# Optimization experiments

Measured on AMD Instinct MI355X. Metric: run time of the kernel, lower is better.

Reference implementation:

```python
import jax, jax.numpy as jnp
import numpy as np

B, S, HID = 8, 1024, 1024
NH, HD = 16, 64  # num heads, head dim
EPS = 1e-12


def setup_inputs() -> dict:
    key = jax.random.key(0)
    ks = jax.random.split(key, 8)
    sc = 0.02
    return {
        "hidden_states": jax.random.normal(ks[0], (B, S, HID), jnp.float32),
        "attention_mask": jnp.zeros((B, 1, 1, S), jnp.bool_),
        "rel_pos": jax.random.normal(ks[1], (1, NH, S, S), jnp.float32),
        "rel_2d_pos": jax.random.normal(ks[2], (1, NH, S, S), jnp.float32),
        "w_qkv": jax.random.normal(ks[3], (3 * HID, HID), jnp.float32) * sc,
        "q_bias": jnp.zeros((1, 1, HID), jnp.float32),
        "v_bias": jnp.zeros((1, 1, HID), jnp.float32),
        "w_out": jax.random.normal(ks[4], (HID, HID), jnp.float32) * sc,
        "b_out": jnp.zeros((HID,), jnp.float32),
        "ln_gamma": jnp.ones((HID,), jnp.float32),
        "ln_beta": jnp.zeros((HID,), jnp.float32),
    }


def reference(hidden_states, attention_mask, rel_pos, rel_2d_pos,
              w_qkv, q_bias, v_bias, w_out, b_out, ln_gamma, ln_beta):
    x = hidden_states
    # fast_qkv: single projection, no bias; then add q_bias/v_bias
    qkv = jnp.einsum('bsh,oh->bso', x, w_qkv)  # [B,S,3*HID]
    q, k, v = jnp.split(qkv, 3, axis=-1)
    q = q + q_bias
    v = v + v_bias
    # [B,S,HID] -> [B,NH,S,HD]
    to_heads = lambda t: t.reshape(B, S, NH, HD).transpose(0, 2, 1, 3)
    qh, kh, vh = to_heads(q), to_heads(k), to_heads(v)
    qh = qh / jnp.sqrt(jnp.float32(HD))
    scores = jnp.einsum('bhqd,bhkd->bhqk', qh, kh)
    scores = scores + rel_pos + rel_2d_pos
    scores = jnp.where(attention_mask, -jnp.inf, scores.astype(jnp.float32))
    probs = jax.nn.softmax(scores, axis=-1).astype(vh.dtype)
    ctx = jnp.einsum('bhqk,bhkd->bhqd', probs, vh)
    ctx = ctx.transpose(0, 2, 1, 3).reshape(B, S, HID)
    # self-output: dense + residual + LayerNorm
    h = jnp.einsum('bsh,oh->bso', ctx, w_out) + b_out + x
    mu = jnp.mean(h, axis=-1, keepdims=True)
    var = jnp.var(h, axis=-1, keepdims=True)
    out = (h - mu) / jnp.sqrt(var + EPS) * ln_gamma + ln_beta
    return out
```

## Files before the change

### kernel.cpp

```cpp
#include <hip/hip_runtime.h>
#include <stdint.h>
#include <stddef.h>

typedef unsigned short u16;
typedef __attribute__((ext_vector_type(8))) short short8;
typedef __attribute__((ext_vector_type(4))) float f32x4;
typedef __attribute__((ext_vector_type(4))) unsigned short ushort4v;
typedef __attribute__((ext_vector_type(4))) unsigned char uchar4v;
typedef __attribute__((ext_vector_type(2))) unsigned int uint2v;

constexpr int B_ = 8, S_ = 1024, HID_ = 1024, NH_ = 16, HD_ = 64;
#define LOG2E_F 1.4426950408889634f
#define QSCALE_F 0.18033688011112043f
#define SHIFT2_F 11.541560327111707f

__device__ __forceinline__ u16 f2b(float f) {
  unsigned int u = __builtin_bit_cast(unsigned int, f);
  u += 0x7fff + ((u >> 16) & 1);
  return (u16)(u >> 16);
}
__device__ __forceinline__ float b2f(u16 s) {
  unsigned int u = ((unsigned int)s) << 16;
  return __builtin_bit_cast(float, u);
}
__device__ __forceinline__ float fexp2(float x) {
#if __has_builtin(__builtin_amdgcn_exp2f)
  return __builtin_amdgcn_exp2f(x);
#else
  return exp2f(x);
#endif
}
__device__ __forceinline__ void llds16(const void* g, void* l) {
  __builtin_amdgcn_global_load_lds((__attribute__((address_space(1))) void*)g,
                                   (__attribute__((address_space(3))) void*)l, 16, 0, 0);
}

__global__ __launch_bounds__(256) void prep_cvt(
    const float* __restrict__ x, const float* __restrict__ wqkv,
    const float* __restrict__ wout, u16* __restrict__ xb,
    u16* __restrict__ wqkvb, u16* __restrict__ woutb) {
  const int NX8 = B_ * S_ * HID_ / 8, NW18 = 3 * HID_ * HID_ / 8, NW28 = HID_ * HID_ / 8;
  const int tot = NX8 + NW18 + NW28;
  for (int i = blockIdx.x * blockDim.x + threadIdx.x; i < tot; i += gridDim.x * blockDim.x) {
    const float4* s; u16* d; int j;
    if (i < NX8)              { s = (const float4*)x;    d = xb;    j = i; }
    else if (i < NX8 + NW18)  { s = (const float4*)wqkv; d = wqkvb; j = i - NX8; }
    else                      { s = (const float4*)wout; d = woutb; j = i - NX8 - NW18; }
    float4 v0 = s[2 * (size_t)j], v1 = s[2 * (size_t)j + 1];
    short8 o;
    o[0] = (short)f2b(v0.x); o[1] = (short)f2b(v0.y);
    o[2] = (short)f2b(v0.z); o[3] = (short)f2b(v0.w);
    o[4] = (short)f2b(v1.x); o[5] = (short)f2b(v1.y);
    o[6] = (short)f2b(v1.z); o[7] = (short)f2b(v1.w);
    *(short8*)(d + 8 * (size_t)j) = o;
  }
}

__global__ __launch_bounds__(256) void gemm_qkv(
    const u16* __restrict__ W, const u16* __restrict__ X,
    const float* __restrict__ qbias, const float* __restrict__ vbias,
    u16* __restrict__ Qb, u16* __restrict__ Kb, u16* __restrict__ Vtb) {
  constexpr int K = HID_;
  __shared__ u16 smem[128 * 136];
  u16* Ws0 = smem;
  u16* Ws1 = smem + 4096;
  u16* Xs0 = smem + 8192;
  u16* Xs1 = smem + 12288;
  const int lin = blockIdx.x;
  const int virt = (lin & 7) * 192 + (lin >> 3);
  const int o0 = (virt % 24) * 128, s0 = (virt / 24) * 128;
  const int t = threadIdx.x, lane = t & 63, wv = t >> 6;
  const int wr = wv >> 1, wc = wv & 1, ln = lane & 15, q8 = lane >> 4;
  f32x4 acc[4][4] = {};

  for (int kt = 0; kt < K / 64; ++kt) {
    const int k0 = kt * 64;
#pragma unroll
    for (int c = 0; c < 2; ++c) {
      int idx = c * 256 + t, row = idx >> 2, cc = (idx & 3) * 8;
      const int db = (c * 256 + wv * 64) * 8;
      llds16(W + (size_t)(o0 + row) * K + k0 + cc,      Ws0 + db);
      llds16(W + (size_t)(o0 + row) * K + k0 + 32 + cc, Ws1 + db);
      llds16(X + (size_t)(s0 + row) * K + k0 + cc,      Xs0 + db);
      llds16(X + (size_t)(s0 + row) * K + k0 + 32 + cc, Xs1 + db);
    }
    __syncthreads();
#pragma unroll
    for (int hh = 0; hh < 2; ++hh) {
      const u16* Wh = hh ? Ws1 : Ws0;
      const u16* Xh = hh ? Xs1 : Xs0;
      short8 of[4], sf[4];
#pragma unroll
      for (int mi = 0; mi < 4; ++mi)
        of[mi] = *(const short8*)(Wh + (wr * 64 + mi * 16 + ln) * 32 + q8 * 8);
#pragma unroll
      for (int ni = 0; ni < 4; ++ni)
        sf[ni] = *(const short8*)(Xh + (wc * 64 + ni * 16 + ln) * 32 + q8 * 8);
#pragma unroll
      for (int mi = 0; mi < 4; ++mi)
#pragma unroll
        for (int ni = 0; ni < 4; ++ni)
          acc[mi][ni] = __builtin_amdgcn_mfma_f32_16x16x32_bf16(of[mi], sf[ni], acc[mi][ni], 0, 0, 0);
    }
    __syncthreads();
  }

  const int sec = o0 >> 10;

  if (sec == 2) {
#pragma unroll
    for (int mi = 0; mi < 4; ++mi) {
      const int ocol = wr * 64 + mi * 16 + q8 * 4;
      const int oo = (o0 + ocol) & 1023;
      float4 b4 = *(const float4*)(vbias + oo);
#pragma unroll
      for (int ni = 0; ni < 4; ++ni) {
        const int srow = wc * 64 + ni * 16 + ln;
#pragma unroll
        for (int r = 0; r < 4; ++r)
          smem[(ocol + r) * 136 + srow] = f2b(acc[mi][ni][r] + ((const float*)&b4)[r]);
      }
    }
    __syncthreads();
#pragma unroll
    for (int i = 0; i < 8; ++i) {
      int flat = i * 256 + t;
      int dl = flat >> 4, s8 = (flat & 15) * 8;
      short8 v = *(const short8*)(smem + dl * 136 + s8);
      int oo = (o0 + dl) & 1023, hh = oo >> 6, dd = oo & 63;
      int bb = s0 >> 10, ss = (s0 + s8) & 1023;
      *(short8*)(Vtb + ((size_t)(bb * NH_ + hh) * HD_ + dd) * S_ + ss) = v;
    }
    return;
  }

#pragma unroll
  for (int mi = 0; mi < 4; ++mi) {
    const int ocol = wr * 64 + mi * 16 + q8 * 4;
    const int oo = (o0 + ocol) & 1023;
    float4 b4;
    if (sec == 0) b4 = *(const float4*)(qbias + oo);
    else          b4 = float4{0.f, 0.f, 0.f, 0.f};
#pragma unroll
    for (int ni = 0; ni < 4; ++ni) {
      const int srow = wc * 64 + ni * 16 + ln;
      u16 e[4];
#pragma unroll
      for (int r = 0; r < 4; ++r) {
        float v = acc[mi][ni][r] + ((const float*)&b4)[r];
        if (sec == 0) v *= QSCALE_F;
        e[r] = f2b(v);
      }
      uint2v pw;
      pw[0] = (unsigned)e[0] | ((unsigned)e[1] << 16);
      pw[1] = (unsigned)e[2] | ((unsigned)e[3] << 16);
      *(uint2v*)(smem + srow * 136 + ocol) = pw;
    }
  }
  __syncthreads();
  u16* dst = (sec == 0) ? Qb : Kb;
#pragma unroll
  for (int i = 0; i < 8; ++i) {
    int flat = i * 256 + t;
    int srow = flat >> 4, c8 = (flat & 15) * 8;
    short8 v = *(const short8*)(smem + srow * 136 + c8);
    int oo = (o0 + c8) & 1023, hh = oo >> 6, dd = oo & 63;
    int s = s0 + srow, bb = s >> 10, ss = s & 1023;
    *(short8*)(dst + ((size_t)(bb * NH_ + hh) * S_ + ss) * HD_ + dd) = v;
  }
}

__global__ __launch_bounds__(512, 2) void flash_attn(
    const u16* __restrict__ Qb, const u16* __restrict__ Kb,
    const u16* __restrict__ Vtb, const float* __restrict__ relp,
    const float* __restrict__ rel2,
    const unsigned char* __restrict__ mask, u16* __restrict__ ctxb) {
  const int lin = blockIdx.x;
  const int virt = (lin & 7) * 64 + (lin >> 3);
  const int h = virt >> 5, qt_blk = (virt >> 3) & 3, b = virt & 7;
  const int bh = b * NH_ + h, q0 = qt_blk * 256;
  const int t = threadIdx.x, lane = t & 63, wv = t >> 6;
  const int ln = lane & 15, q8 = lane >> 4;

  __shared__ u16 smem[28160];
  u16* Ks  = smem;
  u16* Vts = smem + 9216;
  u16* Pw  = smem + 17920 + wv * 1280;

  const int krow = t >> 3, kcol = (t & 7) * 8;
  const int vrow = t >> 4, vcol = (t & 15) * 8;

  const float* relA = relp + ((size_t)h * S_ + q0 + wv * 32 + ln) * S_;
  const float* relB = rel2 + ((size_t)h * S_ + q0 + wv * 32 + ln) * S_;

  short8 kreg[2], vreg[2];
#pragma unroll
  for (int i = 0; i < 2; ++i)
    kreg[i] = *(const short8*)(Kb + ((size_t)bh * S_ + i * 64 + krow) * HD_ + kcol);
#pragma unroll
  for (int i = 0; i < 2; ++i)
    vreg[i] = *(const short8*)(Vtb + ((size_t)bh * HD_ + i * 32 + vrow) * S_ + vcol);

  short8 qf[2][2];
#pragma unroll
  for (int qt = 0; qt < 2; ++qt)
#pragma unroll
    for (int kc = 0; kc < 2; ++kc)
      qf[qt][kc] = *(const short8*)(Qb + ((size_t)bh * S_ + q0 + wv * 32 + qt * 16 + ln) * HD_ + kc * 32 + q8 * 8);

  f32x4 Oa[4][2] = {};
  float rs2[2] = {0.f, 0.f};

  for (int kt128 = 0; kt128 < 8; ++kt128) {
    const int k0 = kt128 * 128;

    uchar4v mg[4][2];
#pragma unroll
    for (int kvc = 0; kvc < 4; ++kvc)
#pragma unroll
      for (int sub = 0; sub < 2; ++sub)
        mg[kvc][sub] = *(const uchar4v*)(mask + b * S_ + k0 + (kvc * 2 + sub) * 16 + q8 * 4);

    __syncthreads();
#pragma unroll
    for (int i = 0; i < 2; ++i)
      *(short8*)(Ks + (i * 64 + krow) * 72 + kcol) = kreg[i];
#pragma unroll
    for (int i = 0; i < 2; ++i)
      *(short8*)(Vts + (i * 32 + vrow) * 136 + vcol) = vreg[i];
    if (kt128 < 7) {
      const int k0n = k0 + 128;
#pragma unroll
      for (int i = 0; i < 2; ++i)
        kreg[i] = *(const short8*)(Kb + ((size_t)bh * S_ + k0n + i * 64 + krow) * HD_ + kcol);
#pragma unroll
      for (int i = 0; i < 2; ++i)
        vreg[i] = *(const short8*)(Vtb + ((size_t)bh * HD_ + i * 32 + vrow) * S_ + k0n + vcol);
    }
    __syncthreads();

#pragma unroll
    for (int kvc = 0; kvc < 4; ++kvc) {
#pragma unroll
      for (int sub = 0; sub < 2; ++sub) {
        const int kt = kvc * 2 + sub;
        const int kg = k0 + kt * 16 + q8 * 4;
        short8 kf0 = *(const short8*)(Ks + (kt * 16 + ln) * 72 + q8 * 8);
        short8 kf1 = *(const short8*)(Ks + (kt * 16 + ln) * 72 + 32 + q8 * 8);
        uchar4v m4 = mg[kvc][sub];
        f32x4 mbase;
#pragma unroll
        for (int r = 0; r < 4; ++r) mbase[r] = (m4[r] ? -1e30f : 0.f) - SHIFT2_F;
#pragma unroll
        for (int qt = 0; qt < 2; ++qt) {
          float4 ra = *(const float4*)(relA + (size_t)(qt * 16) * S_ + kg);
          float4 rb = *(const float4*)(relB + (size_t)(qt * 16) * S_ + kg);
          f32x4 sc;
          sc[0] = (ra.x + rb.x) * LOG2E_F + mbase[0];
          sc[1] = (ra.y + rb.y) * LOG2E_F + mbase[1];
          sc[2] = (ra.z + rb.z) * LOG2E_F + mbase[2];
          sc[3] = (ra.w + rb.w) * LOG2E_F + mbase[3];
          sc = __builtin_amdgcn_mfma_f32_16x16x32_bf16(kf0, qf[qt][0], sc, 0, 0, 0);
          sc = __builtin_amdgcn_mfma_f32_16x16x32_bf16(kf1, qf[qt][1], sc, 0, 0, 0);
          float p0 = fexp2(sc[0]), p1 = fexp2(sc[1]);
          float p2 = fexp2(sc[2]), p3 = fexp2(sc[3]);
          rs2[qt] += (p0 + p1) + (p2 + p3);
          uint2v pw;
          pw[0] = (unsigned)f2b(p0) | ((unsigned)f2b(p1) << 16);
          pw[1] = (unsigned)f2b(p2) | ((unsigned)f2b(p3) << 16);
          *(uint2v*)(Pw + (qt * 16 + ln) * 40 + sub * 16 + q8 * 4) = pw;
        }
      }
      short8 pf0 = *(const short8*)(Pw + ln * 40 + q8 * 8);
      short8 pf1 = *(const short8*)(Pw + (16 + ln) * 40 + q8 * 8);
#pragma unroll
      for (int mt = 0; mt < 4; ++mt) {
        short8 vf = *(const short8*)(Vts + (mt * 16 + ln) * 136 + kvc * 32 + q8 * 8);
        Oa[mt][0] = __builtin_amdgcn_mfma_f32_16x16x32_bf16(vf, pf0, Oa[mt][0], 0, 0, 0);
        Oa[mt][1] = __builtin_amdgcn_mfma_f32_16x16x32_bf16(vf, pf1, Oa[mt][1], 0, 0, 0);
      }
    }
  }

  float inv[2];
#pragma unroll
  for (int qt = 0; qt < 2; ++qt) {
    rs2[qt] += __shfl_xor(rs2[qt], 16, 64);
    rs2[qt] += __shfl_xor(rs2[qt], 32, 64);
    inv[qt] = 1.f / rs2[qt];
  }

  __syncthreads();
  u16* Ob = smem + wv * 2304;
#pragma unroll
  for (int qt = 0; qt < 2; ++qt)
#pragma unroll
    for (int mt = 0; mt < 4; ++mt) {
      u16 e[4];
#pragma unroll
      for (int r = 0; r < 4; ++r) e[r] = f2b(Oa[mt][qt][r] * inv[qt]);
      uint2v pw;
      pw[0] = (unsigned)e[0] | ((unsigned)e[1] << 16);
      pw[1] = (unsigned)e[2] | ((unsigned)e[3] << 16);
      *(uint2v*)(Ob + (qt * 16 + ln) * 72 + mt * 16 + q8 * 4) = pw;
    }
#pragma unroll
  for (int p = 0; p < 4; ++p) {
    int row = p * 8 + (lane >> 3);
    int c8 = (lane & 7) * 8;
    short8 v = *(const short8*)(Ob + row * 72 + c8);
    int q = q0 + wv * 32 + row;
    *(short8*)(ctxb + ((size_t)(b * S_ + q)) * HID_ + h * 64 + c8) = v;
  }
}

__global__ __launch_bounds__(256) void gemm_out(
    const u16* __restrict__ W, const u16* __restrict__ X,
    const float* __restrict__ bout, const float* __restrict__ xres,
    u16* __restrict__ hb) {
  constexpr int K = HID_;
  __shared__ u16 smem[128 * 136];
  u16* Ws0 = smem;
  u16* Ws1 = smem + 4096;
  u16* Xs0 = smem + 8192;
  u16* Xs1 = smem + 12288;
  const int lin = blockIdx.x;
  const int virt = (lin & 7) * 64 + (lin >> 3);
  const int o0 = (virt % 8) * 128, s0 = (virt / 8) * 128;
  const int t = threadIdx.x, lane = t & 63, wv = t >> 6;
  const int wr = wv >> 1, wc = wv & 1, ln = lane & 15, q8 = lane >> 4;
  f32x4 acc[4][4] = {};

  for (int kt = 0; kt < K / 64; ++kt) {
    const int k0 = kt * 64;
#pragma unroll
    for (int c = 0; c < 2; ++c) {
      int idx = c * 256 + t, row = idx >> 2, cc = (idx & 3) * 8;
      const int db = (c * 256 + wv * 64) * 8;
      llds16(W + (size_t)(o0 + row) * K + k0 + cc,      Ws0 + db);
      llds16(W + (size_t)(o0 + row) * K + k0 + 32 + cc, Ws1 + db);
      llds16(X + (size_t)(s0 + row) * K + k0 + cc,      Xs0 + db);
      llds16(X + (size_t)(s0 + row) * K + k0 + 32 + cc, Xs1 + db);
    }
    __syncthreads();
#pragma unroll
    for (int hh = 0; hh < 2; ++hh) {
      const u16* Wh = hh ? Ws1 : Ws0;
      const u16* Xh = hh ? Xs1 : Xs0;
      short8 of[4], sf[4];
#pragma unroll
      for (int mi = 0; mi < 4; ++mi)
        of[mi] = *(const short8*)(Wh + (wr * 64 + mi * 16 + ln) * 32 + q8 * 8);
#pragma unroll
      for (int ni = 0; ni < 4; ++ni)
        sf[ni] = *(const short8*)(Xh + (wc * 64 + ni * 16 + ln) * 32 + q8 * 8);
#pragma unroll
      for (int mi = 0; mi < 4; ++mi)
#pragma unroll
        for (int ni = 0; ni < 4; ++ni)
          acc[mi][ni] = __builtin_amdgcn_mfma_f32_16x16x32_bf16(of[mi], sf[ni], acc[mi][ni], 0, 0, 0);
    }
    __syncthreads();
  }

#pragma unroll
  for (int mi = 0; mi < 4; ++mi) {
    const int ocol = wr * 64 + mi * 16 + q8 * 4;
    float4 b4 = *(const float4*)(bout + o0 + ocol);
#pragma unroll
    for (int ni = 0; ni < 4; ++ni) {
      const int srow = wc * 64 + ni * 16 + ln;
      u16 e[4];
#pragma unroll
      for (int r = 0; r < 4; ++r) e[r] = f2b(acc[mi][ni][r] + ((const float*)&b4)[r]);
      uint2v pw;
      pw[0] = (unsigned)e[0] | ((unsigned)e[1] << 16);
      pw[1] = (unsigned)e[2] | ((unsigned)e[3] << 16);
      *(uint2v*)(smem + srow * 136 + ocol) = pw;
    }
  }
  __syncthreads();
#pragma unroll
  for (int i = 0; i < 8; ++i) {
    int flat = i * 256 + t;
    int srow = flat >> 4, c8 = (flat & 15) * 8;
    short8 v = *(const short8*)(smem + srow * 136 + c8);
    int s = s0 + srow, o = o0 + c8;
    float4 x0 = *(const float4*)(xres + (size_t)s * HID_ + o);
    float4 x1 = *(const float4*)(xres + (size_t)s * HID_ + o + 4);
    short8 st;
#pragma unroll
    for (int j = 0; j < 4; ++j) st[j] = (short)f2b(b2f((u16)v[j]) + ((const float*)&x0)[j]);
#pragma unroll
    for (int j = 0; j < 4; ++j) st[4 + j] = (short)f2b(b2f((u16)v[4 + j]) + ((const float*)&x1)[j]);
    *(short8*)(hb + (size_t)s * HID_ + o) = st;
  }
}

__global__ __launch_bounds__(256) void ln_kernel(
    const u16* __restrict__ hb, const float* __restrict__ gamma,
    const float* __restrict__ beta, float* __restrict__ out) {
  __shared__ float red[8];
  const int t = threadIdx.x, lane = t & 63, wv = t >> 6;
  const int row = blockIdx.x;
  const u16* hr = hb + (size_t)row * HID_;
  ushort4v a = *(const ushort4v*)(hr + t * 4);
  float v[4];
#pragma unroll
  for (int j = 0; j < 4; ++j) v[j] = b2f(a[j]);
  float sum = (v[0] + v[1]) + (v[2] + v[3]);
  float sq = (v[0] * v[0] + v[1] * v[1]) + (v[2] * v[2] + v[3] * v[3]);
#pragma unroll
  for (int off = 1; off < 64; off <<= 1) {
    sum += __shfl_xor(sum, off, 64);
    sq  += __shfl_xor(sq, off, 64);
  }
  if (lane == 0) { red[wv] = sum; red[4 + wv] = sq; }
  __syncthreads();
  const float s4 = (red[0] + red[1]) + (red[2] + red[3]);
  const float q4 = (red[4] + red[5]) + (red[6] + red[7]);
  const float mu = s4 * (1.f / HID_);
  const float var = q4 * (1.f / HID_) - mu * mu;
  const float inv = 1.f / sqrtf(var + 1e-12f);
  float4 g = *(const float4*)(gamma + t * 4);
  float4 be = *(const float4*)(beta + t * 4);
  float4 o;
  o.x = (v[0] - mu) * inv * g.x + be.x;
  o.y = (v[1] - mu) * inv * g.y + be.y;
  o.z = (v[2] - mu) * inv * g.z + be.z;
  o.w = (v[3] - mu) * inv * g.w + be.w;
  *(float4*)(out + (size_t)row * HID_ + t * 4) = o;
}

extern "C" void kernel_launch(void* const* d_in, const int* in_sizes, int n_in,
                              void* d_out, int out_size, void* d_ws, size_t ws_size,
                              hipStream_t stream) {
  (void)in_sizes; (void)n_in; (void)out_size; (void)ws_size;
  const float* x     = (const float*)d_in[0];
  const unsigned char* mask = (const unsigned char*)d_in[1];
  const float* relp  = (const float*)d_in[2];
  const float* rel2  = (const float*)d_in[3];
  const float* wqkv  = (const float*)d_in[4];
  const float* qbias = (const float*)d_in[5];
  const float* vbias = (const float*)d_in[6];
  const float* wout  = (const float*)d_in[7];
  const float* bout  = (const float*)d_in[8];
  const float* gamma = (const float*)d_in[9];
  const float* beta  = (const float*)d_in[10];
  float* out = (float*)d_out;

  char* ws = (char*)d_ws;
  const size_t MB = (size_t)1 << 20;
  u16* xb    = (u16*)(ws + 0 * MB);
  u16* wqkvb = (u16*)(ws + 16 * MB);
  u16* woutb = (u16*)(ws + 22 * MB);
  u16* Qb    = (u16*)(ws + 56 * MB);
  u16* Kb    = (u16*)(ws + 72 * MB);
  u16* Vtb   = (u16*)(ws + 88 * MB);
  u16* ctxb  = (u16*)(ws + 104 * MB);
  u16* hb    = (u16*)(ws + 120 * MB);

  prep_cvt<<<2048, 256, 0, stream>>>(x, wqkv, wout, xb, wqkvb, woutb);
  gemm_qkv<<<1536, 256, 0, stream>>>(wqkvb, xb, qbias, vbias, Qb, Kb, Vtb);
  flash_attn<<<512, 512, 0, stream>>>(Qb, Kb, Vtb, relp, rel2, mask, ctxb);
  gemm_out<<<512, 256, 0, stream>>>(woutb, ctxb, bout, x, hb);
  ln_kernel<<<8192, 256, 0, stream>>>(hb, gamma, beta, out);
}
```

Measured before the change: 447.8 us.

## Precombine relative-position biases into permuted bf16 tile layout before attention

A new pre-pass kernel sums the two fp32 relative-position bias tensors, scales them by log2(e), rounds to bf16, and writes them in a layout matching the MFMA accumulator fragments of the attention kernel. The attention kernel then reads one compact bf16 stream instead of two fp32 streams, and prefetches it one chunk ahead in registers. This targets the attention kernel's dominant bias read traffic: bias data is shared across the batch but was re-read as fp32 for every batch. The cost is an extra kernel launch with its own read/write pass, and bf16 rounding of the bias before softmax.

```diff
diff --git a/kernel.cpp b/kernel.cpp
--- a/kernel.cpp
+++ b/kernel.cpp
@@ -56,6 +56,33 @@
   }
 }
 
+__global__ __launch_bounds__(256) void rel_perm(
+    const float* __restrict__ a, const float* __restrict__ b, u16* __restrict__ relb) {
+  __shared__ u16 lbuf[16 * 1032];
+  const int qtg = blockIdx.x, h = blockIdx.y;
+  const int t = threadIdx.x;
+#pragma unroll
+  for (int it = 0; it < 16; ++it) {
+    int idx = it * 256 + t;
+    int lq = idx >> 8, kc = idx & 255;
+    size_t src = ((size_t)h * S_ + qtg * 16 + lq) * S_ + kc * 4;
+    float4 va = *(const float4*)(a + src);
+    float4 vb = *(const float4*)(b + src);
+    ushort4v o;
+    o[0] = f2b((va.x + vb.x) * LOG2E_F); o[1] = f2b((va.y + vb.y) * LOG2E_F);
+    o[2] = f2b((va.z + vb.z) * LOG2E_F); o[3] = f2b((va.w + vb.w) * LOG2E_F);
+    *(ushort4v*)(lbuf + lq * 1032 + kc * 4) = o;
+  }
+  __syncthreads();
+#pragma unroll
+  for (int it = 0; it < 16; ++it) {
+    int c = it * 16 + (t >> 4);
+    int ktg = c >> 2, qk = c & 3, lq = t & 15;
+    ushort4v v = *(const ushort4v*)(lbuf + lq * 1032 + ktg * 16 + qk * 4);
+    *(ushort4v*)(relb + ((((size_t)h * 64 + ktg) * 64 + qtg) * 4 + qk) * 64 + lq * 4) = v;
+  }
+}
+
 __global__ __launch_bounds__(256) void gemm_qkv(
     const u16* __restrict__ W, const u16* __restrict__ X,
     const float* __restrict__ qbias, const float* __restrict__ vbias,
@@ -172,8 +199,7 @@
 
 __global__ __launch_bounds__(512, 2) void flash_attn(
     const u16* __restrict__ Qb, const u16* __restrict__ Kb,
-    const u16* __restrict__ Vtb, const float* __restrict__ relp,
-    const float* __restrict__ rel2,
+    const u16* __restrict__ Vtb, const u16* __restrict__ relb,
     const unsigned char* __restrict__ mask, u16* __restrict__ ctxb) {
   const int lin = blockIdx.x;
   const int virt = (lin & 7) * 64 + (lin >> 3);
@@ -190,8 +216,8 @@
   const int krow = t >> 3, kcol = (t & 7) * 8;
   const int vrow = t >> 4, vcol = (t & 15) * 8;
 
-  const float* relA = relp + ((size_t)h * S_ + q0 + wv * 32 + ln) * S_;
-  const float* relB = rel2 + ((size_t)h * S_ + q0 + wv * 32 + ln) * S_;
+  const u16* relbase = relb + (((size_t)h * 64) * 64 + (size_t)(qt_blk * 16 + wv * 2)) * 4 * 64
+                            + (size_t)q8 * 64 + ln * 4;
 
   short8 kreg[2], vreg[2];
 #pragma unroll
@@ -220,6 +246,14 @@
 #pragma unroll
       for (int sub = 0; sub < 2; ++sub)
         mg[kvc][sub] = *(const uchar4v*)(mask + b * S_ + k0 + (kvc * 2 + sub) * 16 + q8 * 4);
+
+    ushort4v relg[4][2][2];
+#pragma unroll
+    for (int sub = 0; sub < 2; ++sub)
+#pragma unroll
+      for (int qt = 0; qt < 2; ++qt)
+        relg[0][sub][qt] = *(const ushort4v*)(relbase +
+            (((size_t)(kt128 * 8 + sub) * 64 + qt) * 4) * 64);
 
     __syncthreads();
 #pragma unroll
@@ -241,10 +275,17 @@
 
 #pragma unroll
     for (int kvc = 0; kvc < 4; ++kvc) {
+      if (kvc < 3) {
+#pragma unroll
+        for (int sub = 0; sub < 2; ++sub)
+#pragma unroll
+          for (int qt = 0; qt < 2; ++qt)
+            relg[kvc + 1][sub][qt] = *(const ushort4v*)(relbase +
+                (((size_t)(kt128 * 8 + (kvc + 1) * 2 + sub) * 64 + qt) * 4) * 64);
+      }
 #pragma unroll
       for (int sub = 0; sub < 2; ++sub) {
         const int kt = kvc * 2 + sub;
-        const int kg = k0 + kt * 16 + q8 * 4;
         short8 kf0 = *(const short8*)(Ks + (kt * 16 + ln) * 72 + q8 * 8);
         short8 kf1 = *(const short8*)(Ks + (kt * 16 + ln) * 72 + 32 + q8 * 8);
         uchar4v m4 = mg[kvc][sub];
@@ -253,13 +294,10 @@
         for (int r = 0; r < 4; ++r) mbase[r] = (m4[r] ? -1e30f : 0.f) - SHIFT2_F;
 #pragma unroll
         for (int qt = 0; qt < 2; ++qt) {
-          float4 ra = *(const float4*)(relA + (size_t)(qt * 16) * S_ + kg);
-          float4 rb = *(const float4*)(relB + (size_t)(qt * 16) * S_ + kg);
+          ushort4v r4 = relg[kvc][sub][qt];
           f32x4 sc;
-          sc[0] = (ra.x + rb.x) * LOG2E_F + mbase[0];
-          sc[1] = (ra.y + rb.y) * LOG2E_F + mbase[1];
-          sc[2] = (ra.z + rb.z) * LOG2E_F + mbase[2];
-          sc[3] = (ra.w + rb.w) * LOG2E_F + mbase[3];
+#pragma unroll
+          for (int r = 0; r < 4; ++r) sc[r] = b2f(r4[r]) + mbase[r];
           sc = __builtin_amdgcn_mfma_f32_16x16x32_bf16(kf0, qf[qt][0], sc, 0, 0, 0);
           sc = __builtin_amdgcn_mfma_f32_16x16x32_bf16(kf1, qf[qt][1], sc, 0, 0, 0);
           float p0 = fexp2(sc[0]), p1 = fexp2(sc[1]);
@@ -454,6 +492,7 @@
   u16* xb    = (u16*)(ws + 0 * MB);
   u16* wqkvb = (u16*)(ws + 16 * MB);
   u16* woutb = (u16*)(ws + 22 * MB);
+  u16* relb  = (u16*)(ws + 24 * MB);
   u16* Qb    = (u16*)(ws + 56 * MB);
   u16* Kb    = (u16*)(ws + 72 * MB);
   u16* Vtb   = (u16*)(ws + 88 * MB);
@@ -461,8 +500,9 @@
   u16* hb    = (u16*)(ws + 120 * MB);
 
   prep_cvt<<<2048, 256, 0, stream>>>(x, wqkv, wout, xb, wqkvb, woutb);
+  rel_perm<<<dim3(64, 16), 256, 0, stream>>>(relp, rel2, relb);
   gemm_qkv<<<1536, 256, 0, stream>>>(wqkvb, xb, qbias, vbias, Qb, Kb, Vtb);
-  flash_attn<<<512, 512, 0, stream>>>(Qb, Kb, Vtb, relp, rel2, mask, ctxb);
+  flash_attn<<<512, 512, 0, stream>>>(Qb, Kb, Vtb, relb, mask, ctxb);
   gemm_out<<<512, 256, 0, stream>>>(woutb, ctxb, bout, x, hb);
   ln_kernel<<<8192, 256, 0, stream>>>(hb, gamma, beta, out);
 }
```

Result: faster. 389.0 us (-13.1%).
